# Optimization experiments

Measured on AMD Instinct MI355X. Metric: run time of the kernel, lower is better.

## Reference

```python
import jax, jax.numpy as jnp
import numpy as np

N_HEADS = 16
D_EMBED = 1024
BATCH = 1
SEQ = 4096


def setup_inputs() -> dict:
    key = jax.random.key(0)
    ks = jax.random.split(key, 5)
    d = D_EMBED
    x = jax.random.normal(ks[0], (BATCH, SEQ, d), dtype=jnp.float32)
    # torch Linear weights stored as (in, out) so y = x @ W + b
    W_in = jax.random.normal(ks[1], (d, 3 * d), dtype=jnp.float32) / np.sqrt(d)
    b_in = jax.random.normal(ks[2], (3 * d,), dtype=jnp.float32) * 0.02
    W_out = jax.random.normal(ks[3], (d, d), dtype=jnp.float32) / np.sqrt(d)
    b_out = jax.random.normal(ks[4], (d,), dtype=jnp.float32) * 0.02
    return {"x": x, "W_in": W_in, "b_in": b_in, "W_out": W_out, "b_out": b_out}


def reference(x, W_in, b_in, W_out, b_out):
    B, S, d = x.shape
    H = N_HEADS
    dh = d // H
    qkv = x @ W_in + b_in                      # [B, S, 3d]
    q, k, v = jnp.split(qkv, 3, axis=-1)       # each [B, S, d]
    # [B, S, H, dh] -> [B, H, S, dh]
    q = q.reshape(B, S, H, dh).transpose(0, 2, 1, 3)
    k = k.reshape(B, S, H, dh).transpose(0, 2, 1, 3)
    v = v.reshape(B, S, H, dh).transpose(0, 2, 1, 3)
    scores = jnp.einsum("bhqd,bhkd->bhqk", q, k) / jnp.sqrt(jnp.float32(dh))
    causal = jnp.tril(jnp.ones((S, S), dtype=bool))  # True = keep
    scores = jnp.where(causal, scores, -jnp.inf)
    attn = jax.nn.softmax(scores, axis=-1)
    out = jnp.einsum("bhqk,bhkd->bhqd", attn, v)     # [B, H, S, dh]
    out = out.transpose(0, 2, 1, 3).reshape(B, S, d)
    return out @ W_out + b_out
```

## Files before the change

### kernel.cpp

```cpp
#include <hip/hip_runtime.h>
#include <stdint.h>

#define S_LEN 4096
#define D_EMB 1024
#define NH 16
#define DHEAD 64
#define N3 3072

typedef __attribute__((ext_vector_type(8))) short short8;
typedef __attribute__((ext_vector_type(4))) short short4v;
typedef __attribute__((ext_vector_type(4))) float f32x4;

#define OFF_XB    0u
#define OFF_WINT  4194304u
#define OFF_WOUTT 7340032u
#define OFF_Q     8388608u
#define OFF_ATTN  20971520u

#define QSCALE 0.1803368801111204f
#define DEFER_THR 11.0f

__device__ __forceinline__ unsigned short f2bf(float f) {
  unsigned u = __float_as_uint(f);
  unsigned r = u + 0x7FFFu + ((u >> 16) & 1u);
  return (unsigned short)(r >> 16);
}
__device__ __forceinline__ unsigned cvtpk_bf16(float lo, float hi) {
  unsigned r;
  asm("v_cvt_pk_bf16_f32 %0, %1, %2" : "=v"(r) : "v"(lo), "v"(hi));
  return r;
}
__device__ __forceinline__ void gload16(const void* g, void* l) {
  __builtin_amdgcn_global_load_lds((const __attribute__((address_space(1))) void*)g,
                                   (__attribute__((address_space(3))) void*)l, 16, 0, 0);
}

__global__ __launch_bounds__(256) void prep_kernel(const float* __restrict__ x,
                                                   const float* __restrict__ W_in,
                                                   const float* __restrict__ W_out,
                                                   ushort* __restrict__ xb,
                                                   ushort* __restrict__ wint,
                                                   ushort* __restrict__ woutt) {
  __shared__ float tile[32][33];
  int b = blockIdx.x;
  if (b < 4096) {
    int i = (b * 256 + threadIdx.x) * 4;
    float4 v = *(const float4*)(x + i);
    ushort4 o;
    o.x = f2bf(v.x); o.y = f2bf(v.y); o.z = f2bf(v.z); o.w = f2bf(v.w);
    *(ushort4*)(xb + i) = o;
    return;
  }
  const float* src;
  ushort* dst;
  int R, C, bx, by;
  if (b < 7168) {
    int t = b - 4096;
    src = W_in; dst = wint; R = D_EMB; C = N3;
    bx = t % 96; by = t / 96;
  } else {
    int t = b - 7168;
    src = W_out; dst = woutt; R = D_EMB; C = D_EMB;
    bx = t & 31; by = t >> 5;
  }
  int tx = threadIdx.x & 31, ty = threadIdx.x >> 5;
  int c0 = bx * 32, r0 = by * 32;
#pragma unroll
  for (int i = 0; i < 32; i += 8)
    tile[ty + i][tx] = src[(size_t)(r0 + ty + i) * C + c0 + tx];
  __syncthreads();
#pragma unroll
  for (int i = 0; i < 32; i += 8)
    dst[(size_t)(c0 + ty + i) * R + r0 + tx] = f2bf(tile[tx][ty + i]);
}

__global__ __launch_bounds__(512, 2) void gemm1_8phase(const ushort* __restrict__ A,
                                                       const ushort* __restrict__ Bt,
                                                       const float* __restrict__ bias,
                                                       ushort* __restrict__ o16) {
  __shared__ ushort L[65536];
  const int K = 1024;
  int tid = threadIdx.x, w = tid >> 6, lane = tid & 63;
  int wr = w >> 2, wc = w & 3;
  int l15 = lane & 15, g = lane >> 4;
  int lr = lane >> 3, lc = lane & 7;
  int swcol = (lc ^ lr) * 8;
  int rxor = (l15 & 7) << 3;
  int id = blockIdx.y * 12 + blockIdx.x;
  int id2 = (id & 7) * 24 + (id >> 3);
  int bm = (id2 / 12) * 256, bn = (id2 % 12) * 256;

  f32x4 acc[8][4];
#pragma unroll
  for (int m = 0; m < 8; ++m)
#pragma unroll
    for (int n = 0; n < 4; ++n) acc[m][n] = (f32x4){0.f, 0.f, 0.f, 0.f};

  auto stageA = [&](int t, int h) {
#pragma unroll
    for (int r2 = 0; r2 < 2; ++r2)
      gload16(A + (size_t)(bm + h * 128 + r2 * 64 + w * 8 + lr) * K + t * 64 + swcol,
              &L[((t & 1) * 2 + h) * 8192 + r2 * 4096 + w * 512]);
  };
  auto stageB = [&](int t, int h) {
#pragma unroll
    for (int r2 = 0; r2 < 2; ++r2)
      gload16(Bt + (size_t)(bn + h * 128 + r2 * 64 + w * 8 + lr) * K + t * 64 + swcol,
              &L[32768 + ((t & 1) * 2 + h) * 8192 + r2 * 4096 + w * 512]);
  };

  short8 bf[4][2], af[2][2];
  auto readB = [&](int tb) {
    int base = 32768 + (tb * 2 + (wc >> 1)) * 8192 + (wc & 1) * 4096;
#pragma unroll
    for (int n = 0; n < 4; ++n)
#pragma unroll
      for (int ks = 0; ks < 2; ++ks)
        bf[n][ks] = *(const short8*)&L[base + (n * 16 + l15) * 64 + ((ks * 32 + g * 8) ^ rxor)];
  };
  auto readA2 = [&](int tb, int m0) {
    int base = (tb * 2 + wr) * 8192;
#pragma unroll
    for (int mi = 0; mi < 2; ++mi)
#pragma unroll
      for (int ks = 0; ks < 2; ++ks)
        af[mi][ks] = *(const short8*)&L[base + ((m0 + mi) * 16 + l15) * 64 + ((ks * 32 + g * 8) ^ rxor)];
  };
  auto mfma8 = [&](int m0) {
#pragma unroll
    for (int mi = 0; mi < 2; ++mi)
#pragma unroll
      for (int n = 0; n < 4; ++n)
#pragma unroll
        for (int ks = 0; ks < 2; ++ks)
          acc[m0 + mi][n] =
              __builtin_amdgcn_mfma_f32_16x16x32_bf16(af[mi][ks], bf[n][ks], acc[m0 + mi][n], 0, 0, 0);
  };

#define BAR() __builtin_amdgcn_s_barrier()
#define LGK0() asm volatile("s_waitcnt lgkmcnt(0)" ::: "memory")
#define VM4() asm volatile("s_waitcnt vmcnt(4)" ::: "memory")
#define VM0() asm volatile("s_waitcnt vmcnt(0)" ::: "memory")

  stageA(0, 0); stageA(0, 1); stageB(0, 0); stageB(0, 1);
  stageB(1, 0); stageB(1, 1);
  VM4();
  BAR();

  for (int i = 0; i < 8; ++i) {
    int T = 2 * i;
    bool more = (T + 2 < 16);
    readB(0); readA2(0, 0); stageA(T + 1, 0);
    BAR(); LGK0();
    __builtin_amdgcn_s_setprio(1); mfma8(0); __builtin_amdgcn_s_setprio(0);
    BAR();
    readA2(0, 2); stageA(T + 1, 1);
    BAR(); LGK0();
    __builtin_amdgcn_s_setprio(1); mfma8(2); __builtin_amdgcn_s_setprio(0);
    BAR();
    readA2(0, 4); if (more) stageB(T + 2, 0);
    BAR(); LGK0();
    __builtin_amdgcn_s_setprio(1); mfma8(4); __builtin_amdgcn_s_setprio(0);
    BAR();
    readA2(0, 6); if (more) stageB(T + 2, 1);
    BAR(); LGK0();
    __builtin_amdgcn_s_setprio(1); mfma8(6); __builtin_amdgcn_s_setprio(0);
    if (more) VM4(); else VM0();
    BAR();
    readB(1); readA2(1, 0); if (more) stageA(T + 2, 0);
    BAR(); LGK0();
    __builtin_amdgcn_s_setprio(1); mfma8(0); __builtin_amdgcn_s_setprio(0);
    BAR();
    readA2(1, 2); if (more) stageA(T + 2, 1);
    BAR(); LGK0();
    __builtin_amdgcn_s_setprio(1); mfma8(2); __builtin_amdgcn_s_setprio(0);
    BAR();
    readA2(1, 4); if (more) stageB(T + 3, 0);
    BAR(); LGK0();
    __builtin_amdgcn_s_setprio(1); mfma8(4); __builtin_amdgcn_s_setprio(0);
    BAR();
    readA2(1, 6); if (more) stageB(T + 3, 1);
    BAR(); LGK0();
    __builtin_amdgcn_s_setprio(1); mfma8(6); __builtin_amdgcn_s_setprio(0);
    if (more) VM4(); else VM0();
    BAR();
  }
#undef BAR
#undef LGK0
#undef VM4
#undef VM0

#pragma unroll
  for (int m = 0; m < 8; ++m) {
    int rbase = bm + wr * 128 + m * 16 + g * 4;
#pragma unroll
    for (int n = 0; n < 4; ++n) {
      int c = bn + wc * 64 + n * 16 + l15;
      float bv = bias[c];
      int which = c >> 10, cc = c & 1023, hh = cc >> 6, dcol = cc & 63;
      if (which == 2) {
        ushort4 o;
        o.x = f2bf(acc[m][n][0] + bv);
        o.y = f2bf(acc[m][n][1] + bv);
        o.z = f2bf(acc[m][n][2] + bv);
        o.w = f2bf(acc[m][n][3] + bv);
        *(ushort4*)&o16[8388608u + (size_t)hh * (DHEAD * (size_t)S_LEN) +
                        (size_t)dcol * S_LEN + rbase] = o;
      } else {
        float qs = (which == 0) ? QSCALE : 1.0f;
        ushort* dst = o16 + (size_t)which * 4194304u +
                      (size_t)hh * (S_LEN * DHEAD) + dcol;
#pragma unroll
        for (int j = 0; j < 4; ++j)
          dst[(size_t)(rbase + j) * DHEAD] = f2bf((acc[m][n][j] + bv) * qs);
      }
    }
  }
}

#define BK 64

__global__ __launch_bounds__(256) void gemm2_kernel(const ushort* __restrict__ A,
                                                    const ushort* __restrict__ Bt,
                                                    const float* __restrict__ bias,
                                                    float* __restrict__ o32,
                                                    int N, int K) {
  __shared__ ushort As[128 * 64];
  __shared__ ushort Bs[64 * 64];
  int tid = threadIdx.x, w = tid >> 6, lane = tid & 63;
  int wr = w >> 1, wc = w & 1;
  int l15 = lane & 15, g = lane >> 4;
  int gx = gridDim.x;
  int id = blockIdx.y * gx + blockIdx.x;
  int q8 = (gx * gridDim.y) >> 3;
  int id2 = (id & 7) * q8 + (id >> 3);
  int bm = (id2 / gx) * 128, bn = (id2 % gx) * 64;
  f32x4 acc[4][2];
#pragma unroll
  for (int m = 0; m < 4; ++m)
#pragma unroll
    for (int n = 0; n < 2; ++n) acc[m][n] = (f32x4){0.f, 0.f, 0.f, 0.f};

  int srow = lane >> 3;
  int scol = (lane & 7) * 8;

  for (int k0 = 0; k0 < K; k0 += BK) {
    __syncthreads();
#pragma unroll
    for (int i = 0; i < 4; ++i) {
      int ch = w * 4 + i;
      gload16(A + (size_t)(bm + ch * 8 + srow) * K + k0 + scol, &As[ch * 512]);
    }
#pragma unroll
    for (int i = 0; i < 2; ++i) {
      int ch = w * 2 + i;
      gload16(Bt + (size_t)(bn + ch * 8 + srow) * K + k0 + scol, &Bs[ch * 512]);
    }
    __syncthreads();
    short8 a[4][2], b[2][2];
#pragma unroll
    for (int m = 0; m < 4; ++m)
#pragma unroll
      for (int t = 0; t < 2; ++t)
        a[m][t] = *(const short8*)&As[(wr * 64 + m * 16 + l15) * 64 + t * 32 + g * 8];
#pragma unroll
    for (int n = 0; n < 2; ++n)
#pragma unroll
      for (int t = 0; t < 2; ++t)
        b[n][t] = *(const short8*)&Bs[(wc * 32 + n * 16 + l15) * 64 + t * 32 + g * 8];
#pragma unroll
    for (int m = 0; m < 4; ++m)
#pragma unroll
      for (int n = 0; n < 2; ++n)
#pragma unroll
        for (int t = 0; t < 2; ++t)
          acc[m][n] = __builtin_amdgcn_mfma_f32_16x16x32_bf16(a[m][t], b[n][t], acc[m][n], 0, 0, 0);
  }

#pragma unroll
  for (int m = 0; m < 4; ++m) {
    int rbase = bm + wr * 64 + m * 16 + g * 4;
#pragma unroll
    for (int n = 0; n < 2; ++n) {
      int c = bn + wc * 32 + n * 16 + l15;
      float bv = bias[c];
#pragma unroll
      for (int j = 0; j < 4; ++j)
        o32[(size_t)(rbase + j) * N + c] = acc[m][n][j] + bv;
    }
  }
}

__global__ __launch_bounds__(512) void attn_kernel(const ushort* __restrict__ Q,
                                                   const ushort* __restrict__ Kg,
                                                   const ushort* __restrict__ Vtg,
                                                   ushort* __restrict__ O) {
  __shared__ ushort Ks[2][64 * 64];
  __shared__ ushort Vs[2][64 * 64];
  int bid = blockIdx.x;
  int h = bid & 15;
  int qt = (bid < 256) ? (31 - (bid >> 4)) : ((bid - 256) >> 4);
  int q0 = qt * 128;
  int tid = threadIdx.x, w = tid >> 6, lane = tid & 63;
  int l15 = lane & 15, g = lane >> 4;
  const ushort* qh = Q + (size_t)h * (S_LEN * DHEAD);
  const ushort* kh = Kg + (size_t)h * (S_LEN * DHEAD);
  const ushort* vh = Vtg + (size_t)h * (DHEAD * (size_t)S_LEN);
  int sr = tid >> 3;
  int scc = (tid & 7) * 8;
  int wo = sr * 64 + (((scc * 2) ^ ((sr & 7) << 4)) >> 1);
  int kxor = (l15 & 7) << 4;
  int koff0 = ((g * 16) ^ kxor) >> 1;
  int koff1 = ((64 + g * 16) ^ kxor) >> 1;
  int voff[4];
#pragma unroll
  for (int ct = 0; ct < 4; ++ct) voff[ct] = ((ct * 32 + g * 8) ^ kxor) >> 1;

  int qrow = q0 + w * 16 + l15;
  short8 aq[2];
#pragma unroll
  for (int t = 0; t < 2; ++t)
    aq[t] = *(const short8*)&qh[(size_t)qrow * DHEAD + t * 32 + g * 8];

  f32x4 acc_o[4];
#pragma unroll
  for (int dt = 0; dt < 4; ++dt) acc_o[dt] = (f32x4){0.f, 0.f, 0.f, 0.f};
  float m = -1e30f, l = 0.f;
  int last = 2 * qt + 1;

  {
    short8 ka = *(const short8*)&kh[(size_t)sr * DHEAD + scc];
    short8 va = *(const short8*)&vh[(size_t)sr * S_LEN + scc];
    *(short8*)&Ks[0][wo] = ka;
    *(short8*)&Vs[0][wo] = va;
  }
  short8 nk, nv;
  {
    nk = *(const short8*)&kh[(size_t)(64 + sr) * DHEAD + scc];
    nv = *(const short8*)&vh[(size_t)sr * S_LEN + 64 + scc];
  }
  __syncthreads();
  int cur = 0;

  for (int it = 0; it <= last; ++it) {
    int kv0 = it * 64;
    bool more = (it < last);
    const ushort* Kc = Ks[cur];
    const ushort* Vc = Vs[cur];

    f32x4 accs[4];
#pragma unroll
    for (int ct = 0; ct < 4; ++ct) accs[ct] = (f32x4){0.f, 0.f, 0.f, 0.f};
    __builtin_amdgcn_s_setprio(1);
#pragma unroll
    for (int ct = 0; ct < 4; ++ct) {
      int rb = (ct * 16 + l15) * 64;
      short8 kf0 = *(const short8*)&Kc[rb + koff0];
      short8 kf1 = *(const short8*)&Kc[rb + koff1];
      accs[ct] = __builtin_amdgcn_mfma_f32_16x16x32_bf16(kf0, aq[0], accs[ct], 0, 0, 0);
      accs[ct] = __builtin_amdgcn_mfma_f32_16x16x32_bf16(kf1, aq[1], accs[ct], 0, 0, 0);
    }
    __builtin_amdgcn_s_setprio(0);

    if (it >= 2 * qt) {
#pragma unroll
      for (int ct = 0; ct < 4; ++ct) {
        int kbase = kv0 + ct * 16 + g * 4;
#pragma unroll
        for (int j = 0; j < 4; ++j)
          if (kbase + j > qrow) accs[ct][j] = -1e30f;
      }
    }

    float a0 = fmaxf(fmaxf(accs[0][0], accs[0][1]), fmaxf(accs[0][2], accs[0][3]));
    float a1 = fmaxf(fmaxf(accs[1][0], accs[1][1]), fmaxf(accs[1][2], accs[1][3]));
    float a2 = fmaxf(fmaxf(accs[2][0], accs[2][1]), fmaxf(accs[2][2], accs[2][3]));
    float a3 = fmaxf(fmaxf(accs[3][0], accs[3][1]), fmaxf(accs[3][2], accs[3][3]));
    float pm = fmaxf(fmaxf(a0, a1), fmaxf(a2, a3));

    if (!__all(pm <= m + DEFER_THR)) {
      pm = fmaxf(pm, __shfl_xor(pm, 16));
      pm = fmaxf(pm, __shfl_xor(pm, 32));
      float mnew = fmaxf(m, pm);
      float corr = __builtin_amdgcn_exp2f(m - mnew);
      l *= corr; m = mnew;
#pragma unroll
      for (int dt = 0; dt < 4; ++dt)
#pragma unroll
        for (int j = 0; j < 4; ++j) acc_o[dt][j] *= corr;
    }

    float rs = 0.f;
    short8 pk8[2];
#pragma unroll
    for (int t2 = 0; t2 < 2; ++t2) {
      float p0 = __builtin_amdgcn_exp2f(accs[2 * t2][0] - m);
      float p1 = __builtin_amdgcn_exp2f(accs[2 * t2][1] - m);
      float p2 = __builtin_amdgcn_exp2f(accs[2 * t2][2] - m);
      float p3 = __builtin_amdgcn_exp2f(accs[2 * t2][3] - m);
      float p4 = __builtin_amdgcn_exp2f(accs[2 * t2 + 1][0] - m);
      float p5 = __builtin_amdgcn_exp2f(accs[2 * t2 + 1][1] - m);
      float p6 = __builtin_amdgcn_exp2f(accs[2 * t2 + 1][2] - m);
      float p7 = __builtin_amdgcn_exp2f(accs[2 * t2 + 1][3] - m);
      rs += ((p0 + p1) + (p2 + p3)) + ((p4 + p5) + (p6 + p7));
      union { unsigned u[4]; short8 v; } pu;
      pu.u[0] = cvtpk_bf16(p0, p1);
      pu.u[1] = cvtpk_bf16(p2, p3);
      pu.u[2] = cvtpk_bf16(p4, p5);
      pu.u[3] = cvtpk_bf16(p6, p7);
      pk8[t2] = pu.v;
    }
    l += rs;

    __builtin_amdgcn_s_setprio(1);
#pragma unroll
    for (int dt = 0; dt < 4; ++dt) {
      int rb = (dt * 16 + l15) * 64;
#pragma unroll
      for (int t2 = 0; t2 < 2; ++t2) {
        union { short4v hh[2]; short8 v; } vu;
        vu.hh[0] = *(const short4v*)&Vc[rb + voff[2 * t2]];
        vu.hh[1] = *(const short4v*)&Vc[rb + voff[2 * t2 + 1]];
        acc_o[dt] = __builtin_amdgcn_mfma_f32_16x16x32_bf16(vu.v, pk8[t2], acc_o[dt], 0, 0, 0);
      }
    }
    __builtin_amdgcn_s_setprio(0);

    if (more) {
      *(short8*)&Ks[cur ^ 1][wo] = nk;
      *(short8*)&Vs[cur ^ 1][wo] = nv;
      if (it + 2 <= last) {
        int kv2 = kv0 + 128;
        nk = *(const short8*)&kh[(size_t)(kv2 + sr) * DHEAD + scc];
        nv = *(const short8*)&vh[(size_t)sr * S_LEN + kv2 + scc];
      }
    }
    __syncthreads();
    cur ^= 1;
  }

  l += __shfl_xor(l, 16);
  l += __shfl_xor(l, 32);
  float rl = (l > 0.f) ? 1.f / l : 0.f;
#pragma unroll
  for (int dt = 0; dt < 4; ++dt) {
    ushort4 o;
    o.x = f2bf(acc_o[dt][0] * rl);
    o.y = f2bf(acc_o[dt][1] * rl);
    o.z = f2bf(acc_o[dt][2] * rl);
    o.w = f2bf(acc_o[dt][3] * rl);
    *(ushort4*)&O[(size_t)qrow * D_EMB + h * DHEAD + dt * 16 + g * 4] = o;
  }
}

extern "C" void kernel_launch(void* const* d_in, const int* in_sizes, int n_in,
                              void* d_out, int out_size, void* d_ws, size_t ws_size,
                              hipStream_t stream) {
  const float* x = (const float*)d_in[0];
  const float* W_in = (const float*)d_in[1];
  const float* b_in = (const float*)d_in[2];
  const float* W_out = (const float*)d_in[3];
  const float* b_out = (const float*)d_in[4];
  float* out = (float*)d_out;
  ushort* ws = (ushort*)d_ws;

  prep_kernel<<<8192, 256, 0, stream>>>(x, W_in, W_out,
                                        ws + OFF_XB, ws + OFF_WINT, ws + OFF_WOUTT);
  gemm1_8phase<<<dim3(12, 16), 512, 0, stream>>>(
      ws + OFF_XB, ws + OFF_WINT, b_in, ws + OFF_Q);
  attn_kernel<<<512, 512, 0, stream>>>(
      ws + OFF_Q, ws + OFF_Q + 4194304u, ws + OFF_Q + 8388608u, ws + OFF_ATTN);
  gemm2_kernel<<<dim3(16, 32), 256, 0, stream>>>(
      ws + OFF_ATTN, ws + OFF_WOUTT, b_out, out, D_EMB, D_EMB);
}
```

Before: 133.8 us.

## Stage K/V tiles via direct global-to-LDS loads instead of register staging

Replaces the register-staged double buffer for K and V tiles with direct global-to-LDS loads (gload16), issued at the start of each iteration into the other buffer. The swizzle moves from the LDS write address to the global source column so the layout still matches the existing reads. This removes VGPR staging and the LDS store instructions, but shortens prefetch distance from two tiles to one and adds a full vmcnt wait before each barrier.

```diff
diff --git a/kernel.cpp b/kernel.cpp
--- a/kernel.cpp
+++ b/kernel.cpp
@@ -306,9 +306,10 @@
   const ushort* qh = Q + (size_t)h * (S_LEN * DHEAD);
   const ushort* kh = Kg + (size_t)h * (S_LEN * DHEAD);
   const ushort* vh = Vtg + (size_t)h * (DHEAD * (size_t)S_LEN);
-  int sr = tid >> 3;
-  int scc = (tid & 7) * 8;
-  int wo = sr * 64 + (((scc * 2) ^ ((sr & 7) << 4)) >> 1);
+  int srow = w * 8 + (lane >> 3);
+  int sgcol = (((lane & 7) ^ ((lane >> 3) & 7))) * 8;
+  ushort* kdst0 = &Ks[0][w * 512];  ushort* kdst1 = &Ks[1][w * 512];
+  ushort* vdst0 = &Vs[0][w * 512];  ushort* vdst1 = &Vs[1][w * 512];
   int kxor = (l15 & 7) << 4;
   int koff0 = ((g * 16) ^ kxor) >> 1;
   int koff1 = ((64 + g * 16) ^ kxor) >> 1;
@@ -328,17 +329,9 @@
   float m = -1e30f, l = 0.f;
   int last = 2 * qt + 1;
 
-  {
-    short8 ka = *(const short8*)&kh[(size_t)sr * DHEAD + scc];
-    short8 va = *(const short8*)&vh[(size_t)sr * S_LEN + scc];
-    *(short8*)&Ks[0][wo] = ka;
-    *(short8*)&Vs[0][wo] = va;
-  }
-  short8 nk, nv;
-  {
-    nk = *(const short8*)&kh[(size_t)(64 + sr) * DHEAD + scc];
-    nv = *(const short8*)&vh[(size_t)sr * S_LEN + 64 + scc];
-  }
+  gload16(&kh[(size_t)srow * DHEAD + sgcol], kdst0);
+  gload16(&vh[(size_t)srow * S_LEN + sgcol], vdst0);
+  asm volatile("s_waitcnt vmcnt(0)" ::: "memory");
   __syncthreads();
   int cur = 0;
 
@@ -347,6 +340,12 @@
     bool more = (it < last);
     const ushort* Kc = Ks[cur];
     const ushort* Vc = Vs[cur];
+
+    if (more) {
+      int kv1 = kv0 + 64;
+      gload16(&kh[(size_t)(kv1 + srow) * DHEAD + sgcol], cur ? kdst0 : kdst1);
+      gload16(&vh[(size_t)srow * S_LEN + kv1 + sgcol], cur ? vdst0 : vdst1);
+    }
 
     f32x4 accs[4];
 #pragma unroll
@@ -426,15 +425,7 @@
     }
     __builtin_amdgcn_s_setprio(0);
 
-    if (more) {
-      *(short8*)&Ks[cur ^ 1][wo] = nk;
-      *(short8*)&Vs[cur ^ 1][wo] = nv;
-      if (it + 2 <= last) {
-        int kv2 = kv0 + 128;
-        nk = *(const short8*)&kh[(size_t)(kv2 + sr) * DHEAD + scc];
-        nv = *(const short8*)&vh[(size_t)sr * S_LEN + kv2 + scc];
-      }
-    }
+    asm volatile("s_waitcnt vmcnt(0)" ::: "memory");
     __syncthreads();
     cur ^= 1;
   }
```

Result: no change. 134.7 us (+0.7%).
